# Kernel optimization log

Measured on AMD Instinct MI355X. Metric: run time of the kernel, lower is better.

Reference implementation:

```python
import jax, jax.numpy as jnp
import numpy as np

F_DIM = 256; L = 4; B = 1; H = 160; W = 160; FH = 1024; N = B * H * W

def _ln(x, w, b):
    mu = jnp.mean(x, -1, keepdims=True)
    var = jnp.mean(jnp.square(x - mu), -1, keepdims=True)
    return (x - mu) * jax.lax.rsqrt(var + 1e-5) * w + b

def _conv(x, w, b, groups=1, pad=0):
    y = jax.lax.conv_general_dilated(x, w, (1, 1), [(pad, pad), (pad, pad)],
                                     dimension_numbers=('NCHW', 'OIHW', 'NCHW'),
                                     feature_group_count=groups)
    return y + b[None, :, None, None]

def _wsilu(x):
    return jax.nn.sigmoid(4.0 * x) * x

def setup_inputs() -> dict:
    key = jax.random.key(0)
    ks = iter(jax.random.split(key, 40))
    nk = lambda: next(ks)
    s = 1.0 / np.sqrt(F_DIM).astype(np.float32)
    inp = {}
    inp['x'] = jax.random.normal(nk(), (B, 1, H, W), jnp.float32)
    inp['cin_w1'] = jax.random.normal(nk(), (F_DIM, 1, 1, 1), jnp.float32)
    inp['cin_b1'] = jnp.zeros((F_DIM,), jnp.float32)
    inp['cin_w2'] = jax.random.normal(nk(), (F_DIM, 1, 7, 7), jnp.float32) * 0.15
    inp['cin_b2'] = jnp.zeros((F_DIM,), jnp.float32)
    inp['ln0_w'] = jnp.ones((F_DIM,), jnp.float32); inp['ln0_b'] = jnp.zeros((F_DIM,), jnp.float32)
    inp['ln1_w'] = jnp.ones((L, F_DIM), jnp.float32); inp['ln1_b'] = jnp.zeros((L, F_DIM), jnp.float32)
    inp['ln2_w'] = jnp.ones((L, F_DIM), jnp.float32); inp['ln2_b'] = jnp.zeros((L, F_DIM), jnp.float32)
    for n in ['att_tmk', 'att_tmv', 'att_tmr', 'ffn_tmk', 'ffn_tmr']:
        inp[n] = jax.random.uniform(nk(), (L, F_DIM), jnp.float32)
    inp['att_tf'] = jax.random.normal(nk(), (L, F_DIM), jnp.float32) * 0.5
    # time_decay is stored as -exp(raw) by the module's loader
    inp['att_td'] = -jnp.exp(jax.random.normal(nk(), (L, F_DIM), jnp.float32) * 0.5)
    for n in ['att_kw', 'att_vw', 'att_rw', 'att_ow', 'ffn_rw']:
        inp[n] = jax.random.normal(nk(), (L, F_DIM, F_DIM), jnp.float32) * s
    inp['ffn_kw'] = jax.random.normal(nk(), (L, FH, F_DIM), jnp.float32) * s
    inp['ffn_vw'] = jax.random.normal(nk(), (L, F_DIM, FH), jnp.float32) * (1.0 / np.sqrt(FH).astype(np.float32))
    inp['spa_dw_w'] = jax.random.normal(nk(), (L, F_DIM, 1, 7, 7), jnp.float32) * 0.15
    inp['spa_dw_b'] = jnp.zeros((L, F_DIM), jnp.float32)
    inp['spa_pw_w'] = jax.random.normal(nk(), (L, F_DIM, F_DIM, 1, 1), jnp.float32) * s
    inp['spa_pw_b'] = jnp.zeros((L, F_DIM), jnp.float32)
    st = jnp.zeros((5 * L, N, F_DIM), jnp.float32)
    st = st.at[4::5].add(-1e30)  # pp slots start at -1e30 as in torch init
    inp['state0'] = st
    return inp

def reference(x, cin_w1, cin_b1, cin_w2, cin_b2, ln0_w, ln0_b, ln1_w, ln1_b,
              ln2_w, ln2_b, att_tmk, att_tmv, att_tmr, att_tf, att_td,
              att_kw, att_vw, att_rw, att_ow, ffn_tmk, ffn_tmr, ffn_kw,
              ffn_vw, ffn_rw, spa_dw_w, spa_dw_b, spa_pw_w, spa_pw_b, state0):
    # conv stem: 1x1 -> depthwise 7x7 -> WSiLU
    d = _conv(x, cin_w1, cin_b1)
    d = _wsilu(_conv(d, cin_w2, cin_b2, groups=F_DIM, pad=3))
    d = d.transpose(0, 2, 3, 1).reshape(N, F_DIM)  # 'b f h w -> (b h w) f'
    for i in range(L):
        if i == 0:
            d = _ln(d, ln0_w, ln0_b)
        # --- SA: single-step RWKV WKV ---
        xs = _ln(d, ln1_w[i], ln1_b[i])
        sp = state0[5 * i + 1]
        aa = state0[5 * i + 2]; bb = state0[5 * i + 3]; pp = state0[5 * i + 4]
        xk = xs * att_tmk[i] + sp * (1 - att_tmk[i])
        xv = xs * att_tmv[i] + sp * (1 - att_tmv[i])
        xr = xs * att_tmr[i] + sp * (1 - att_tmr[i])
        r = jax.nn.sigmoid(xr @ att_rw[i].T)
        k = xk @ att_kw[i].T
        v = xv @ att_vw[i].T
        ww = att_tf[i] + k
        p = jnp.maximum(pp, ww)
        e1 = jnp.exp(pp - p); e2 = jnp.exp(ww - p)
        wkv = (e1 * aa + e2 * v) / (e1 * bb + e2)
        d = d + (r * wkv) @ att_ow[i].T
        # --- FF: squared-relu channel mix ---
        xs = _ln(d, ln2_w[i], ln2_b[i])
        sp = state0[5 * i + 0]
        xk = xs * ffn_tmk[i] + sp * (1 - ffn_tmk[i])
        xr = xs * ffn_tmr[i] + sp * (1 - ffn_tmr[i])
        rr = jax.nn.sigmoid(xr @ ffn_rw[i].T)
        kk = jnp.square(jax.nn.relu(xk @ ffn_kw[i].T))
        d = d + rr * (kk @ ffn_vw[i].T)
        # --- spatial residual block ---
        img = d.reshape(B, H, W, F_DIM).transpose(0, 3, 1, 2)
        img = img + _conv(_conv(img, spa_dw_w[i], spa_dw_b[i], groups=F_DIM, pad=3),
                          spa_pw_w[i], spa_pw_b[i])
        d = img.transpose(0, 2, 3, 1).reshape(N, F_DIM)
    return d.reshape(B, H, W, F_DIM).transpose(0, 3, 1, 2)
```

## Files before the change

kernel.cpp:

```cpp
#include <hip/hip_runtime.h>
#include <hip/hip_bf16.h>
#include <cstdint>
#include <cstddef>

#define F_DIMC 256
#define FHC    1024
#define IMGH   160
#define IMGW   160
#define NTOK   25600
#define NLAY   4

using bf16 = __hip_bfloat16;
typedef __attribute__((ext_vector_type(8))) short bf16x8;
typedef __attribute__((ext_vector_type(4))) float f32x4;

__global__ void cvt_bf16_k(const float* __restrict__ s, bf16* __restrict__ t, int n) {
    int i = blockIdx.x * 256 + threadIdx.x;
    if (i < n) t[i] = __float2bfloat16(s[i]);
}

__global__ void dw_transpose_k(const float* __restrict__ src, float* __restrict__ dst, int n) {
    int i = blockIdx.x * 256 + threadIdx.x;
    if (i < n) {
        int f = i & (F_DIMC - 1);
        int lt = i >> 8;
        int t = lt % 49;
        int l = lt / 49;
        dst[i] = src[((size_t)l * F_DIMC + f) * 49 + t];
    }
}

__global__ __launch_bounds__(256)
void stem_k(const float* __restrict__ x, const float* __restrict__ w1,
            const float* __restrict__ b1, const float* __restrict__ w2,
            const float* __restrict__ b2, float* __restrict__ d)
{
    __shared__ float wt[49][F_DIMC];
    __shared__ float xp[196];
    const int tid = threadIdx.x;
    const int h0 = blockIdx.y * 8, w0 = blockIdx.x * 8;
    for (int idx = tid; idx < 49 * F_DIMC; idx += 256) {
        int t = idx >> 8, f = idx & 255;
        wt[t][f] = w2[f * 49 + t];
    }
    for (int p = tid; p < 196; p += 256) {
        int py = p / 14, px = p % 14;
        int gy = h0 + py - 3, gx = w0 + px - 3;
        xp[p] = ((unsigned)gy < IMGH && (unsigned)gx < IMGW) ? x[gy * IMGW + gx] : 0.f;
    }
    __syncthreads();
    const float w1f = w1[tid], b1f = b1[tid], b2f = b2[tid];
    for (int pi = 0; pi < 64; ++pi) {
        int py = pi >> 3, px = pi & 7;
        float sx = 0.f, sw = 0.f;
        for (int t = 0; t < 49; ++t) {
            int ky = t / 7, kx = t % 7;
            int gy = h0 + py + ky - 3, gx = w0 + px + kx - 3;
            float wv = wt[t][tid];
            if ((unsigned)gy < IMGH && (unsigned)gx < IMGW) {
                sx += xp[(py + ky) * 14 + (px + kx)] * wv;
                sw += wv;
            }
        }
        float u = w1f * sx + b1f * sw + b2f;
        d[(size_t)((h0 + py) * IMGW + (w0 + px)) * F_DIMC + tid] = u / (1.f + __expf(-4.f * u));
    }
}

__device__ __forceinline__ void wave_ln(float* x, const float* __restrict__ w,
                                        const float* __restrict__ b, int lane)
{
    float s = x[0] + x[1] + x[2] + x[3];
    #pragma unroll
    for (int m = 1; m < 64; m <<= 1) s += __shfl_xor(s, m, 64);
    float mu = s * 0.00390625f;
    float t0 = x[0] - mu, t1 = x[1] - mu, t2 = x[2] - mu, t3 = x[3] - mu;
    float v = t0 * t0 + t1 * t1 + t2 * t2 + t3 * t3;
    #pragma unroll
    for (int m = 1; m < 64; m <<= 1) v += __shfl_xor(v, m, 64);
    float inv = rsqrtf(v * 0.00390625f + 1e-5f);
    f32x4 wv = *(const f32x4*)(w + lane * 4);
    f32x4 bv = *(const f32x4*)(b + lane * 4);
    x[0] = t0 * inv * wv[0] + bv[0];
    x[1] = t1 * inv * wv[1] + bv[1];
    x[2] = t2 * inv * wv[2] + bv[2];
    x[3] = t3 * inv * wv[3] + bv[3];
}

union Pack4 { bf16 h[4]; uint2 u; };

template<bool LN0>
__global__ __launch_bounds__(256)
void lnmix_sa_k(float* __restrict__ d, const float* __restrict__ sp,
                const float* __restrict__ ln0w, const float* __restrict__ ln0b,
                const float* __restrict__ lnw, const float* __restrict__ lnb,
                const float* __restrict__ tmk, const float* __restrict__ tmv,
                const float* __restrict__ tmr,
                bf16* __restrict__ xk, bf16* __restrict__ xv, bf16* __restrict__ xr)
{
    const int lane = threadIdx.x & 63;
    const int n = blockIdx.x * 4 + (threadIdx.x >> 6);
    const int base = n * F_DIMC + lane * 4;
    f32x4 dv = *(const f32x4*)(d + base);
    float xo[4] = {dv[0], dv[1], dv[2], dv[3]};
    if (LN0) {
        wave_ln(xo, ln0w, ln0b, lane);
        f32x4 o = {xo[0], xo[1], xo[2], xo[3]};
        *(f32x4*)(d + base) = o;
    }
    float xs[4] = {xo[0], xo[1], xo[2], xo[3]};
    wave_ln(xs, lnw, lnb, lane);
    f32x4 spv = *(const f32x4*)(sp + base);
    f32x4 k4 = *(const f32x4*)(tmk + lane * 4);
    f32x4 v4 = *(const f32x4*)(tmv + lane * 4);
    f32x4 r4 = *(const f32x4*)(tmr + lane * 4);
    Pack4 pk, pv, pr;
    #pragma unroll
    for (int j = 0; j < 4; ++j) {
        pk.h[j] = __float2bfloat16(xs[j] * k4[j] + spv[j] * (1.f - k4[j]));
        pv.h[j] = __float2bfloat16(xs[j] * v4[j] + spv[j] * (1.f - v4[j]));
        pr.h[j] = __float2bfloat16(xs[j] * r4[j] + spv[j] * (1.f - r4[j]));
    }
    *(uint2*)(xk + base) = pk.u;
    *(uint2*)(xv + base) = pv.u;
    *(uint2*)(xr + base) = pr.u;
}

__global__ __launch_bounds__(256)
void lnmix_ff_k(const float* __restrict__ d, const float* __restrict__ sp,
                const float* __restrict__ lnw, const float* __restrict__ lnb,
                const float* __restrict__ tmk, const float* __restrict__ tmr,
                bf16* __restrict__ xk, bf16* __restrict__ xr)
{
    const int lane = threadIdx.x & 63;
    const int n = blockIdx.x * 4 + (threadIdx.x >> 6);
    const int base = n * F_DIMC + lane * 4;
    f32x4 dv = *(const f32x4*)(d + base);
    float xs[4] = {dv[0], dv[1], dv[2], dv[3]};
    wave_ln(xs, lnw, lnb, lane);
    f32x4 spv = *(const f32x4*)(sp + base);
    f32x4 k4 = *(const f32x4*)(tmk + lane * 4);
    f32x4 r4 = *(const f32x4*)(tmr + lane * 4);
    Pack4 pk, pr;
    #pragma unroll
    for (int j = 0; j < 4; ++j) {
        pk.h[j] = __float2bfloat16(xs[j] * k4[j] + spv[j] * (1.f - k4[j]));
        pr.h[j] = __float2bfloat16(xs[j] * r4[j] + spv[j] * (1.f - r4[j]));
    }
    *(uint2*)(xk + base) = pk.u;
    *(uint2*)(xr + base) = pr.u;
}

__global__ __launch_bounds__(256)
void wkv_k(const float* __restrict__ r_, const float* __restrict__ k_,
           const float* __restrict__ v_, const float* __restrict__ aa,
           const float* __restrict__ bb, const float* __restrict__ pp,
           const float* __restrict__ tf, bf16* __restrict__ out)
{
    int i = blockIdx.x * 256 + threadIdx.x;
    int f0 = (i << 2) & (F_DIMC - 1);
    f32x4 r4 = *(const f32x4*)(r_ + (size_t)i * 4);
    f32x4 k4 = *(const f32x4*)(k_ + (size_t)i * 4);
    f32x4 v4 = *(const f32x4*)(v_ + (size_t)i * 4);
    f32x4 a4 = *(const f32x4*)(aa + (size_t)i * 4);
    f32x4 b4 = *(const f32x4*)(bb + (size_t)i * 4);
    f32x4 p4 = *(const f32x4*)(pp + (size_t)i * 4);
    f32x4 t4 = *(const f32x4*)(tf + f0);
    Pack4 po;
    #pragma unroll
    for (int j = 0; j < 4; ++j) {
        float ww = t4[j] + k4[j];
        float p = fmaxf(p4[j], ww);
        float e1 = __expf(p4[j] - p);
        float e2 = __expf(ww - p);
        float wkv = (e1 * a4[j] + e2 * v4[j]) / (e1 * b4[j] + e2);
        po.h[j] = __float2bfloat16(r4[j] * wkv);
    }
    *(uint2*)(out + (size_t)i * 4) = po.u;
}

__global__ __launch_bounds__(256)
void dwconv_k(const float* __restrict__ d, const float* __restrict__ wT,
              const float* __restrict__ bias, bf16* __restrict__ out)
{
    __shared__ float patch[100 * 64];
    __shared__ float wt[49 * 64];
    const int lane = threadIdx.x;
    const int ty = threadIdx.y;
    const int f0 = blockIdx.z * 64;
    const int w0 = blockIdx.x * 4, h0 = blockIdx.y * 4;
    for (int t = ty; t < 49; t += 4) wt[t * 64 + lane] = wT[t * F_DIMC + f0 + lane];
    for (int p = ty; p < 100; p += 4) {
        int py = p / 10, px = p % 10;
        int gy = h0 + py - 3, gx = w0 + px - 3;
        float v = 0.f;
        if ((unsigned)gy < IMGH && (unsigned)gx < IMGW)
            v = d[(size_t)(gy * IMGW + gx) * F_DIMC + f0 + lane];
        patch[p * 64 + lane] = v;
    }
    __syncthreads();
    const float b = bias[f0 + lane];
    for (int pi = ty; pi < 16; pi += 4) {
        int py = pi >> 2, px = pi & 3;
        float acc = b;
        #pragma unroll
        for (int t = 0; t < 49; ++t) {
            int ky = t / 7, kx = t % 7;
            acc += patch[((py + ky) * 10 + (px + kx)) * 64 + lane] * wt[t * 64 + lane];
        }
        out[(size_t)((h0 + py) * IMGW + (w0 + px)) * F_DIMC + f0 + lane] = __float2bfloat16(acc);
    }
}

#define GEMM_BK 64
template<int EPI>
__global__ __launch_bounds__(256)
void gemm_bt(const bf16* __restrict__ A, const bf16* __restrict__ Bw,
             int K, int Nout,
             float* __restrict__ Cf, bf16* __restrict__ Cb,
             const float* __restrict__ aux, const float* __restrict__ bias)
{
    __shared__ __align__(16) bf16 As[128 * GEMM_BK];
    __shared__ __align__(16) bf16 Bs[128 * GEMM_BK];
    const int tid = threadIdx.x;
    const int m0 = blockIdx.x * 128;
    const int n0 = blockIdx.y * 128;
    const int lane = tid & 63;
    const int wave = tid >> 6;
    const int wr = wave >> 1, wc = wave & 1;
    f32x4 acc[4][4];
    #pragma unroll
    for (int m = 0; m < 4; ++m)
        #pragma unroll
        for (int n = 0; n < 4; ++n) acc[m][n] = (f32x4){0.f, 0.f, 0.f, 0.f};

    for (int k0 = 0; k0 < K; k0 += GEMM_BK) {
        #pragma unroll
        for (int s = 0; s < 4; ++s) {
            int e = s * 2048 + tid * 8;
            int row = e >> 6, col = e & 63;
            __builtin_amdgcn_global_load_lds(
                (const __attribute__((address_space(1))) void*)(A + (size_t)(m0 + row) * K + (k0 + col)),
                (__attribute__((address_space(3))) void*)(&As[e]), 16, 0, 0);
        }
        #pragma unroll
        for (int s = 0; s < 4; ++s) {
            int e = s * 2048 + tid * 8;
            int row = e >> 6, col = e & 63;
            __builtin_amdgcn_global_load_lds(
                (const __attribute__((address_space(1))) void*)(Bw + (size_t)(n0 + row) * K + (k0 + col)),
                (__attribute__((address_space(3))) void*)(&Bs[e]), 16, 0, 0);
        }
        __syncthreads();
        #pragma unroll
        for (int kk = 0; kk < GEMM_BK; kk += 32) {
            const int lr = lane & 15;
            const int lk = kk + (lane >> 4) * 8;
            bf16x8 af[4], bfr[4];
            #pragma unroll
            for (int m = 0; m < 4; ++m)
                af[m] = *(const bf16x8*)&As[(wr * 64 + m * 16 + lr) * GEMM_BK + lk];
            #pragma unroll
            for (int n = 0; n < 4; ++n)
                bfr[n] = *(const bf16x8*)&Bs[(wc * 64 + n * 16 + lr) * GEMM_BK + lk];
            #pragma unroll
            for (int m = 0; m < 4; ++m)
                #pragma unroll
                for (int n = 0; n < 4; ++n)
                    acc[m][n] = __builtin_amdgcn_mfma_f32_16x16x32_bf16(af[m], bfr[n], acc[m][n], 0, 0, 0);
        }
        __syncthreads();
    }
    const int lr0 = (lane >> 4) * 4;
    const int lc = lane & 15;
    #pragma unroll
    for (int m = 0; m < 4; ++m) {
        #pragma unroll
        for (int n = 0; n < 4; ++n) {
            #pragma unroll
            for (int j = 0; j < 4; ++j) {
                int row = m0 + wr * 64 + m * 16 + lr0 + j;
                int col = n0 + wc * 64 + n * 16 + lc;
                size_t cidx = (size_t)row * Nout + col;
                float v = acc[m][n][j];
                if constexpr (EPI == 0) Cf[cidx] = v;
                else if constexpr (EPI == 1) Cf[cidx] = 1.f / (1.f + __expf(-v));
                else if constexpr (EPI == 2) { float t = fmaxf(v, 0.f); Cb[cidx] = __float2bfloat16(t * t); }
                else if constexpr (EPI == 3) Cf[cidx] += v;
                else if constexpr (EPI == 4) Cf[cidx] += aux[cidx] * v;
                else if constexpr (EPI == 5) Cf[cidx] += v + bias[col];
            }
        }
    }
}

__global__ __launch_bounds__(256)
void transpose_out_k(const float* __restrict__ d, float* __restrict__ out)
{
    __shared__ float tile[32][33];
    const int n0 = blockIdx.x * 32, f0 = blockIdx.y * 32;
    const int tx = threadIdx.x, ty = threadIdx.y;
    for (int r = ty; r < 32; r += 8) tile[r][tx] = d[(size_t)(n0 + r) * F_DIMC + f0 + tx];
    __syncthreads();
    for (int r = ty; r < 32; r += 8) out[(size_t)(f0 + r) * NTOK + n0 + tx] = tile[tx][r];
}

extern "C" void kernel_launch(void* const* d_in, const int* in_sizes, int n_in,
                              void* d_out, int out_size, void* d_ws, size_t ws_size,
                              hipStream_t stream)
{
    if (n_in < 30) return;
    const float* x        = (const float*)d_in[0];
    const float* cin_w1   = (const float*)d_in[1];
    const float* cin_b1   = (const float*)d_in[2];
    const float* cin_w2   = (const float*)d_in[3];
    const float* cin_b2   = (const float*)d_in[4];
    const float* ln0_w    = (const float*)d_in[5];
    const float* ln0_b    = (const float*)d_in[6];
    const float* ln1_w    = (const float*)d_in[7];
    const float* ln1_b    = (const float*)d_in[8];
    const float* ln2_w    = (const float*)d_in[9];
    const float* ln2_b    = (const float*)d_in[10];
    const float* att_tmk  = (const float*)d_in[11];
    const float* att_tmv  = (const float*)d_in[12];
    const float* att_tmr  = (const float*)d_in[13];
    const float* ffn_tmk  = (const float*)d_in[14];
    const float* ffn_tmr  = (const float*)d_in[15];
    const float* att_tf   = (const float*)d_in[16];
    const float* att_kw   = (const float*)d_in[18];
    const float* att_vw   = (const float*)d_in[19];
    const float* att_rw   = (const float*)d_in[20];
    const float* att_ow   = (const float*)d_in[21];
    const float* ffn_rw   = (const float*)d_in[22];
    const float* ffn_kw   = (const float*)d_in[23];
    const float* ffn_vw   = (const float*)d_in[24];
    const float* spa_dw_w = (const float*)d_in[25];
    const float* spa_dw_b = (const float*)d_in[26];
    const float* spa_pw_w = (const float*)d_in[27];
    const float* spa_pw_b = (const float*)d_in[28];
    const float* state0   = (const float*)d_in[29];
    float* out = (float*)d_out;

    const size_t NF = (size_t)NTOK * F_DIMC;
    char* wsp = (char*)d_ws;
    size_t off = 0;
    auto alloc = [&](size_t bytes) -> void* {
        void* p = wsp + off;
        off += (bytes + 255) & ~(size_t)255;
        return p;
    };
    float* d_buf = (float*)alloc(NF * 4);
    float* Gk    = (float*)alloc(NF * 4);
    float* Gv    = (float*)alloc(NF * 4);
    float* Gr    = (float*)alloc(NF * 4);
    bf16*  xk    = (bf16*)alloc(NF * 2);
    bf16*  xv    = (bf16*)alloc(NF * 2);
    bf16*  xr    = (bf16*)alloc(NF * 2);
    bf16*  ab    = (bf16*)alloc(NF * 2);
    bf16*  kkb   = (bf16*)alloc((size_t)NTOK * FHC * 2);
    const size_t WSQ = (size_t)NLAY * F_DIMC * F_DIMC;
    bf16* kwb  = (bf16*)alloc(WSQ * 2);
    bf16* vwb  = (bf16*)alloc(WSQ * 2);
    bf16* rwb  = (bf16*)alloc(WSQ * 2);
    bf16* owb  = (bf16*)alloc(WSQ * 2);
    bf16* frwb = (bf16*)alloc(WSQ * 2);
    bf16* fkwb = (bf16*)alloc((size_t)NLAY * FHC * F_DIMC * 2);
    bf16* fvwb = (bf16*)alloc((size_t)NLAY * F_DIMC * FHC * 2);
    bf16* pwb  = (bf16*)alloc(WSQ * 2);
    float* dwT = (float*)alloc((size_t)NLAY * 49 * F_DIMC * 4);
    if (off > ws_size) return;

    auto cvt = [&](const float* s, bf16* t, int n) {
        cvt_bf16_k<<<dim3((n + 255) / 256), dim3(256), 0, stream>>>(s, t, n);
    };
    cvt(att_kw, kwb, (int)WSQ);
    cvt(att_vw, vwb, (int)WSQ);
    cvt(att_rw, rwb, (int)WSQ);
    cvt(att_ow, owb, (int)WSQ);
    cvt(ffn_rw, frwb, (int)WSQ);
    cvt(ffn_kw, fkwb, NLAY * FHC * F_DIMC);
    cvt(ffn_vw, fvwb, NLAY * F_DIMC * FHC);
    cvt(spa_pw_w, pwb, (int)WSQ);
    {
        int n = NLAY * 49 * F_DIMC;
        dw_transpose_k<<<dim3((n + 255) / 256), dim3(256), 0, stream>>>(spa_dw_w, dwT, n);
    }

    stem_k<<<dim3(IMGW / 8, IMGH / 8), dim3(256), 0, stream>>>(x, cin_w1, cin_b1, cin_w2, cin_b2, d_buf);

    for (int i = 0; i < NLAY; ++i) {
        const float* sp_ff = state0 + (size_t)(5 * i + 0) * NF;
        const float* sp_at = state0 + (size_t)(5 * i + 1) * NF;
        const float* aa    = state0 + (size_t)(5 * i + 2) * NF;
        const float* bb    = state0 + (size_t)(5 * i + 3) * NF;
        const float* pp    = state0 + (size_t)(5 * i + 4) * NF;
        const float* l1w = ln1_w + i * F_DIMC, *l1b = ln1_b + i * F_DIMC;
        const float* l2w = ln2_w + i * F_DIMC, *l2b = ln2_b + i * F_DIMC;
        const float* tmk = att_tmk + i * F_DIMC, *tmv = att_tmv + i * F_DIMC, *tmr = att_tmr + i * F_DIMC;
        const float* ftmk = ffn_tmk + i * F_DIMC, *ftmr = ffn_tmr + i * F_DIMC;
        const float* tf = att_tf + i * F_DIMC;
        const bf16* kw_i  = kwb  + (size_t)i * F_DIMC * F_DIMC;
        const bf16* vw_i  = vwb  + (size_t)i * F_DIMC * F_DIMC;
        const bf16* rw_i  = rwb  + (size_t)i * F_DIMC * F_DIMC;
        const bf16* ow_i  = owb  + (size_t)i * F_DIMC * F_DIMC;
        const bf16* frw_i = frwb + (size_t)i * F_DIMC * F_DIMC;
        const bf16* fkw_i = fkwb + (size_t)i * FHC * F_DIMC;
        const bf16* fvw_i = fvwb + (size_t)i * F_DIMC * FHC;
        const bf16* pw_i  = pwb  + (size_t)i * F_DIMC * F_DIMC;
        const float* dwT_i = dwT + (size_t)i * 49 * F_DIMC;
        const float* dwb_i = spa_dw_b + i * F_DIMC;
        const float* pwbias_i = spa_pw_b + i * F_DIMC;

        if (i == 0)
            lnmix_sa_k<true><<<dim3(NTOK / 4), dim3(256), 0, stream>>>(
                d_buf, sp_at, ln0_w, ln0_b, l1w, l1b, tmk, tmv, tmr, xk, xv, xr);
        else
            lnmix_sa_k<false><<<dim3(NTOK / 4), dim3(256), 0, stream>>>(
                d_buf, sp_at, ln0_w, ln0_b, l1w, l1b, tmk, tmv, tmr, xk, xv, xr);

        gemm_bt<0><<<dim3(NTOK / 128, 2), dim3(256), 0, stream>>>(xk, kw_i, F_DIMC, F_DIMC, Gk, nullptr, nullptr, nullptr);
        gemm_bt<0><<<dim3(NTOK / 128, 2), dim3(256), 0, stream>>>(xv, vw_i, F_DIMC, F_DIMC, Gv, nullptr, nullptr, nullptr);
        gemm_bt<1><<<dim3(NTOK / 128, 2), dim3(256), 0, stream>>>(xr, rw_i, F_DIMC, F_DIMC, Gr, nullptr, nullptr, nullptr);
        wkv_k<<<dim3((int)(NF / 4 / 256)), dim3(256), 0, stream>>>(Gr, Gk, Gv, aa, bb, pp, tf, ab);
        gemm_bt<3><<<dim3(NTOK / 128, 2), dim3(256), 0, stream>>>(ab, ow_i, F_DIMC, F_DIMC, d_buf, nullptr, nullptr, nullptr);

        lnmix_ff_k<<<dim3(NTOK / 4), dim3(256), 0, stream>>>(d_buf, sp_ff, l2w, l2b, ftmk, ftmr, xk, xr);
        gemm_bt<1><<<dim3(NTOK / 128, 2), dim3(256), 0, stream>>>(xr, frw_i, F_DIMC, F_DIMC, Gr, nullptr, nullptr, nullptr);
        gemm_bt<2><<<dim3(NTOK / 128, 8), dim3(256), 0, stream>>>(xk, fkw_i, F_DIMC, FHC, nullptr, kkb, nullptr, nullptr);
        gemm_bt<4><<<dim3(NTOK / 128, 2), dim3(256), 0, stream>>>(kkb, fvw_i, FHC, F_DIMC, d_buf, nullptr, Gr, nullptr);

        dwconv_k<<<dim3(IMGW / 4, IMGH / 4, 4), dim3(64, 4), 0, stream>>>(d_buf, dwT_i, dwb_i, ab);
        gemm_bt<5><<<dim3(NTOK / 128, 2), dim3(256), 0, stream>>>(ab, pw_i, F_DIMC, F_DIMC, d_buf, nullptr, nullptr, pwbias_i);
    }

    transpose_out_k<<<dim3(NTOK / 32, F_DIMC / 32), dim3(32, 8), 0, stream>>>(d_buf, out);
}
```

Baseline: 2.330 ms.

## Batch weight conversions, fuse k/v/r GEMMs into one launch, retile stem

Merges the eight weight-conversion launches into two batched kernels, and merges the three attention projection GEMMs per layer into one launch indexed by blockIdx.z. The stem convolution is retiled to 64 channels by a 16-pixel row segment, with sliding-window register reuse and a validity flag stored alongside each input pixel. The goal is fewer launches, better GPU fill for the small GEMMs, and a cheaper stem. The stem no longer branches on image borders but does extra FMAs for the weight sum.

```diff
diff --git a/kernel.cpp b/kernel.cpp
--- a/kernel.cpp
+++ b/kernel.cpp
@@ -14,9 +14,17 @@
 typedef __attribute__((ext_vector_type(8))) short bf16x8;
 typedef __attribute__((ext_vector_type(4))) float f32x4;
 
-__global__ void cvt_bf16_k(const float* __restrict__ s, bf16* __restrict__ t, int n) {
+struct Cvt6 { const float* s[6]; bf16* d[6]; };
+__global__ void cvt6_k(Cvt6 a, int n) {
+    int z = blockIdx.y;
     int i = blockIdx.x * 256 + threadIdx.x;
-    if (i < n) t[i] = __float2bfloat16(s[i]);
+    if (i < n) a.d[z][i] = __float2bfloat16(a.s[z][i]);
+}
+struct Cvt2 { const float* s[2]; bf16* d[2]; };
+__global__ void cvt2_k(Cvt2 a, int n) {
+    int z = blockIdx.y;
+    int i = blockIdx.x * 256 + threadIdx.x;
+    if (i < n) a.d[z][i] = __float2bfloat16(a.s[z][i]);
 }
 
 __global__ void dw_transpose_k(const float* __restrict__ src, float* __restrict__ dst, int n) {
@@ -31,39 +39,59 @@
 }
 
 __global__ __launch_bounds__(256)
-void stem_k(const float* __restrict__ x, const float* __restrict__ w1,
-            const float* __restrict__ b1, const float* __restrict__ w2,
-            const float* __restrict__ b2, float* __restrict__ d)
-{
-    __shared__ float wt[49][F_DIMC];
-    __shared__ float xp[196];
+void stem2_k(const float* __restrict__ x, const float* __restrict__ w1,
+             const float* __restrict__ b1, const float* __restrict__ w2,
+             const float* __restrict__ b2, float* __restrict__ d)
+{
+    __shared__ float wts[49][64];
+    __shared__ float w1s[64], b1s[64], b2s[64];
+    __shared__ float2 xp[7][22];
     const int tid = threadIdx.x;
-    const int h0 = blockIdx.y * 8, w0 = blockIdx.x * 8;
-    for (int idx = tid; idx < 49 * F_DIMC; idx += 256) {
-        int t = idx >> 8, f = idx & 255;
-        wt[t][f] = w2[f * 49 + t];
-    }
-    for (int p = tid; p < 196; p += 256) {
-        int py = p / 14, px = p % 14;
-        int gy = h0 + py - 3, gx = w0 + px - 3;
-        xp[p] = ((unsigned)gy < IMGH && (unsigned)gx < IMGW) ? x[gy * IMGW + gx] : 0.f;
+    const int f0 = blockIdx.y * 64;
+    const int y = blockIdx.x / 10;
+    const int x0 = (blockIdx.x % 10) * 16;
+
+    for (int idx = tid; idx < 49 * 64; idx += 256) {
+        int t = idx >> 6, fl = idx & 63;
+        wts[t][fl] = w2[(f0 + fl) * 49 + t];
+    }
+    if (tid < 64) {
+        w1s[tid] = w1[f0 + tid];
+        b1s[tid] = b1[f0 + tid];
+        b2s[tid] = b2[f0 + tid];
+    }
+    for (int p = tid; p < 7 * 22; p += 256) {
+        int py = p / 22, px = p % 22;
+        int gy = y + py - 3, gx = x0 + px - 3;
+        bool ok = (unsigned)gy < IMGH && (unsigned)gx < IMGW;
+        xp[py][px] = ok ? make_float2(x[gy * IMGW + gx], 1.f) : make_float2(0.f, 0.f);
     }
     __syncthreads();
-    const float w1f = w1[tid], b1f = b1[tid], b2f = b2[tid];
-    for (int pi = 0; pi < 64; ++pi) {
-        int py = pi >> 3, px = pi & 7;
-        float sx = 0.f, sw = 0.f;
-        for (int t = 0; t < 49; ++t) {
-            int ky = t / 7, kx = t % 7;
-            int gy = h0 + py + ky - 3, gx = w0 + px + kx - 3;
-            float wv = wt[t][tid];
-            if ((unsigned)gy < IMGH && (unsigned)gx < IMGW) {
-                sx += xp[(py + ky) * 14 + (px + kx)] * wv;
-                sw += wv;
+
+    const int fl = tid & 63;
+    const int xbase = (tid >> 6) * 4;
+    float acc[4] = {0.f, 0.f, 0.f, 0.f}, accw[4] = {0.f, 0.f, 0.f, 0.f};
+    #pragma unroll
+    for (int ky = 0; ky < 7; ++ky) {
+        float2 row[10];
+        #pragma unroll
+        for (int q = 0; q < 10; ++q) row[q] = xp[ky][xbase + q];
+        #pragma unroll
+        for (int kx = 0; kx < 7; ++kx) {
+            float w = wts[ky * 7 + kx][fl];
+            #pragma unroll
+            for (int j = 0; j < 4; ++j) {
+                acc[j]  = fmaf(row[j + kx].x, w, acc[j]);
+                accw[j] = fmaf(row[j + kx].y, w, accw[j]);
             }
         }
-        float u = w1f * sx + b1f * sw + b2f;
-        d[(size_t)((h0 + py) * IMGW + (w0 + px)) * F_DIMC + tid] = u / (1.f + __expf(-4.f * u));
+    }
+    const float w1f = w1s[fl], b1f = b1s[fl], b2f = b2s[fl];
+    #pragma unroll
+    for (int j = 0; j < 4; ++j) {
+        float u = fmaf(w1f, acc[j], fmaf(b1f, accw[j], b2f));
+        int pix = y * IMGW + x0 + xbase + j;
+        d[(size_t)pix * F_DIMC + f0 + fl] = u / (1.f + __expf(-4.f * u));
     }
 }
 
@@ -213,6 +241,84 @@
 }
 
 #define GEMM_BK 64
+
+struct G3 { const bf16* A0; const bf16* A1; const bf16* A2;
+            const bf16* W0; const bf16* W1; const bf16* W2;
+            float* C0; float* C1; float* C2; };
+__global__ __launch_bounds__(256)
+void gemm3_k(G3 g)
+{
+    __shared__ __align__(16) bf16 As[128 * GEMM_BK];
+    __shared__ __align__(16) bf16 Bs[128 * GEMM_BK];
+    const int z = blockIdx.z;
+    const bf16* __restrict__ A  = z == 0 ? g.A0 : z == 1 ? g.A1 : g.A2;
+    const bf16* __restrict__ Bw = z == 0 ? g.W0 : z == 1 ? g.W1 : g.W2;
+    float* __restrict__ C       = z == 0 ? g.C0 : z == 1 ? g.C1 : g.C2;
+    const int tid = threadIdx.x;
+    const int m0 = blockIdx.x * 128;
+    const int n0 = blockIdx.y * 128;
+    const int lane = tid & 63;
+    const int wave = tid >> 6;
+    const int wr = wave >> 1, wc = wave & 1;
+    f32x4 acc[4][4];
+    #pragma unroll
+    for (int m = 0; m < 4; ++m)
+        #pragma unroll
+        for (int n = 0; n < 4; ++n) acc[m][n] = (f32x4){0.f, 0.f, 0.f, 0.f};
+
+    for (int k0 = 0; k0 < F_DIMC; k0 += GEMM_BK) {
+        #pragma unroll
+        for (int s = 0; s < 4; ++s) {
+            int e = s * 2048 + tid * 8;
+            int row = e >> 6, col = e & 63;
+            __builtin_amdgcn_global_load_lds(
+                (const __attribute__((address_space(1))) void*)(A + (size_t)(m0 + row) * F_DIMC + (k0 + col)),
+                (__attribute__((address_space(3))) void*)(&As[e]), 16, 0, 0);
+        }
+        #pragma unroll
+        for (int s = 0; s < 4; ++s) {
+            int e = s * 2048 + tid * 8;
+            int row = e >> 6, col = e & 63;
+            __builtin_amdgcn_global_load_lds(
+                (const __attribute__((address_space(1))) void*)(Bw + (size_t)(n0 + row) * F_DIMC + (k0 + col)),
+                (__attribute__((address_space(3))) void*)(&Bs[e]), 16, 0, 0);
+        }
+        __syncthreads();
+        #pragma unroll
+        for (int kk = 0; kk < GEMM_BK; kk += 32) {
+            const int lr = lane & 15;
+            const int lk = kk + (lane >> 4) * 8;
+            bf16x8 af[4], bfr[4];
+            #pragma unroll
+            for (int m = 0; m < 4; ++m)
+                af[m] = *(const bf16x8*)&As[(wr * 64 + m * 16 + lr) * GEMM_BK + lk];
+            #pragma unroll
+            for (int n = 0; n < 4; ++n)
+                bfr[n] = *(const bf16x8*)&Bs[(wc * 64 + n * 16 + lr) * GEMM_BK + lk];
+            #pragma unroll
+            for (int m = 0; m < 4; ++m)
+                #pragma unroll
+                for (int n = 0; n < 4; ++n)
+                    acc[m][n] = __builtin_amdgcn_mfma_f32_16x16x32_bf16(af[m], bfr[n], acc[m][n], 0, 0, 0);
+        }
+        __syncthreads();
+    }
+    const int lr0 = (lane >> 4) * 4;
+    const int lc = lane & 15;
+    #pragma unroll
+    for (int m = 0; m < 4; ++m)
+        #pragma unroll
+        for (int n = 0; n < 4; ++n)
+            #pragma unroll
+            for (int j = 0; j < 4; ++j) {
+                int row = m0 + wr * 64 + m * 16 + lr0 + j;
+                int col = n0 + wc * 64 + n * 16 + lc;
+                float v = acc[m][n][j];
+                if (z == 2) v = 1.f / (1.f + __expf(-v));
+                C[(size_t)row * F_DIMC + col] = v;
+            }
+}
+
 template<int EPI>
 __global__ __launch_bounds__(256)
 void gemm_bt(const bf16* __restrict__ A, const bf16* __restrict__ Bw,
@@ -283,8 +389,7 @@
                 int col = n0 + wc * 64 + n * 16 + lc;
                 size_t cidx = (size_t)row * Nout + col;
                 float v = acc[m][n][j];
-                if constexpr (EPI == 0) Cf[cidx] = v;
-                else if constexpr (EPI == 1) Cf[cidx] = 1.f / (1.f + __expf(-v));
+                if constexpr (EPI == 1) Cf[cidx] = 1.f / (1.f + __expf(-v));
                 else if constexpr (EPI == 2) { float t = fmaxf(v, 0.f); Cb[cidx] = __float2bfloat16(t * t); }
                 else if constexpr (EPI == 3) Cf[cidx] += v;
                 else if constexpr (EPI == 4) Cf[cidx] += aux[cidx] * v;
@@ -370,23 +475,25 @@
     float* dwT = (float*)alloc((size_t)NLAY * 49 * F_DIMC * 4);
     if (off > ws_size) return;
 
-    auto cvt = [&](const float* s, bf16* t, int n) {
-        cvt_bf16_k<<<dim3((n + 255) / 256), dim3(256), 0, stream>>>(s, t, n);
-    };
-    cvt(att_kw, kwb, (int)WSQ);
-    cvt(att_vw, vwb, (int)WSQ);
-    cvt(att_rw, rwb, (int)WSQ);
-    cvt(att_ow, owb, (int)WSQ);
-    cvt(ffn_rw, frwb, (int)WSQ);
-    cvt(ffn_kw, fkwb, NLAY * FHC * F_DIMC);
-    cvt(ffn_vw, fvwb, NLAY * F_DIMC * FHC);
-    cvt(spa_pw_w, pwb, (int)WSQ);
     {
+        Cvt6 c6;
+        c6.s[0] = att_kw;  c6.d[0] = kwb;
+        c6.s[1] = att_vw;  c6.d[1] = vwb;
+        c6.s[2] = att_rw;  c6.d[2] = rwb;
+        c6.s[3] = att_ow;  c6.d[3] = owb;
+        c6.s[4] = ffn_rw;  c6.d[4] = frwb;
+        c6.s[5] = spa_pw_w; c6.d[5] = pwb;
+        cvt6_k<<<dim3(((int)WSQ + 255) / 256, 6), dim3(256), 0, stream>>>(c6, (int)WSQ);
+        Cvt2 c2;
+        c2.s[0] = ffn_kw; c2.d[0] = fkwb;
+        c2.s[1] = ffn_vw; c2.d[1] = fvwb;
+        int n2 = NLAY * FHC * F_DIMC;
+        cvt2_k<<<dim3((n2 + 255) / 256, 2), dim3(256), 0, stream>>>(c2, n2);
         int n = NLAY * 49 * F_DIMC;
         dw_transpose_k<<<dim3((n + 255) / 256), dim3(256), 0, stream>>>(spa_dw_w, dwT, n);
     }
 
-    stem_k<<<dim3(IMGW / 8, IMGH / 8), dim3(256), 0, stream>>>(x, cin_w1, cin_b1, cin_w2, cin_b2, d_buf);
+    stem2_k<<<dim3(IMGH * 10, 4), dim3(256), 0, stream>>>(x, cin_w1, cin_b1, cin_w2, cin_b2, d_buf);
 
     for (int i = 0; i < NLAY; ++i) {
         const float* sp_ff = state0 + (size_t)(5 * i + 0) * NF;
@@ -418,9 +525,12 @@
             lnmix_sa_k<false><<<dim3(NTOK / 4), dim3(256), 0, stream>>>(
                 d_buf, sp_at, ln0_w, ln0_b, l1w, l1b, tmk, tmv, tmr, xk, xv, xr);
 
-        gemm_bt<0><<<dim3(NTOK / 128, 2), dim3(256), 0, stream>>>(xk, kw_i, F_DIMC, F_DIMC, Gk, nullptr, nullptr, nullptr);
-        gemm_bt<0><<<dim3(NTOK / 128, 2), dim3(256), 0, stream>>>(xv, vw_i, F_DIMC, F_DIMC, Gv, nullptr, nullptr, nullptr);
-        gemm_bt<1><<<dim3(NTOK / 128, 2), dim3(256), 0, stream>>>(xr, rw_i, F_DIMC, F_DIMC, Gr, nullptr, nullptr, nullptr);
+        G3 g3;
+        g3.A0 = xk; g3.A1 = xv; g3.A2 = xr;
+        g3.W0 = kw_i; g3.W1 = vw_i; g3.W2 = rw_i;
+        g3.C0 = Gk; g3.C1 = Gv; g3.C2 = Gr;
+        gemm3_k<<<dim3(NTOK / 128, 2, 3), dim3(256), 0, stream>>>(g3);
+
         wkv_k<<<dim3((int)(NF / 4 / 256)), dim3(256), 0, stream>>>(Gr, Gk, Gv, aa, bb, pp, tf, ab);
         gemm_bt<3><<<dim3(NTOK / 128, 2), dim3(256), 0, stream>>>(ab, ow_i, F_DIMC, F_DIMC, d_buf, nullptr, nullptr, nullptr);
 
```

After: 1.943 ms. 1.2x faster.
